# Kernel optimization log

Measured on AMD Instinct MI355X. Metric: run time of the kernel, lower is better.

## Reference

```python
import jax, jax.numpy as jnp
import numpy as np

NC = 5  # num_clusters == unfold window size


def conv1x3(x, w, b):
    # x: (B, Cin, H, W); w: (Cout, Cin, 1, 3); padding (0,1) like torch Conv2d
    y = jax.lax.conv_general_dilated(
        x, w, window_strides=(1, 1), padding=((0, 0), (1, 1)),
        dimension_numbers=("NCHW", "OIHW", "NCHW"))
    return y + b[None, :, None, None]


def setup_inputs() -> dict:
    key = jax.random.key(0)
    ks = jax.random.split(key, 8)
    b, h, l, d = 8, 8, 1024, 64
    dm = h * d  # d_model = 512
    f32 = jnp.float32
    s_conv1 = 1.0 / np.sqrt(dm * 3)
    s_conv2 = 1.0 / np.sqrt(NC * 3)
    s_lin = 1.0 / np.sqrt(NC)
    return {
        "Q": jax.random.normal(ks[0], (b, h, l, d), f32),
        "K": jax.random.normal(ks[1], (b, h, l, d), f32),
        "V": jax.random.normal(ks[2], (b, h, l, d), f32),
        "w_proj_k": jax.random.normal(ks[3], (NC, dm, 1, 3), f32) * s_conv1,
        "b_proj_k": jnp.zeros((NC,), f32),
        "w_proj_back": jax.random.normal(ks[4], (dm, NC, 1, 3), f32) * s_conv2,
        "b_proj_back": jnp.zeros((dm,), f32),
        "w_ck": jax.random.normal(ks[5], (NC, NC), f32) * s_lin,
        "b_ck": jnp.zeros((NC,), f32),
        "w_cq": jax.random.normal(ks[6], (NC, NC), f32) * s_lin,
        "b_cq": jnp.zeros((NC,), f32),
    }


def reference(Q, K, V, w_proj_k, b_proj_k, w_proj_back, b_proj_back,
              w_ck, b_ck, w_cq, b_cq):
    b, h, l, d = Q.shape
    u = NC  # unfolding window
    # --- padded unfold along batch dim: window i is K_padded[i:i+u] ---
    K_padded = jnp.concatenate(
        [jnp.zeros((u, h, l, d), Q.dtype), K[1:]], axis=0)  # (u+b-1, h, l, d)
    idx = jnp.arange(b)[:, None] + jnp.arange(u)[None, :]     # (b, u)
    Kw = K_padded[idx]                                        # (b, u, h, l, d)
    Kw = jnp.transpose(Kw, (0, 2, 3, 4, 1))                   # (b, h, l, d, u) == torch unfold layout
    K_unfold = Kw.reshape(b, h * d, l, u)                     # raw reshape, matches torch
    # --- project to clusters ---
    ckp = jax.nn.relu(conv1x3(K_unfold, w_proj_k, b_proj_k))  # (b, NC, l, u)
    ckp = jnp.transpose(ckp, (0, 2, 3, 1))                    # (b, l, u, NC)
    cluster_k = jax.nn.softmax(ckp @ w_ck.T + b_ck, axis=-1)
    cluster_q = jax.nn.softmax(ckp @ w_cq.T + b_cq, axis=-1)
    # --- distributional loss ---
    mu = jnp.mean(cluster_q, axis=-1)                         # (b, l, u)
    sigma = jax.nn.softplus(jnp.std(cluster_q, axis=-1, ddof=1))  # unbiased std like torch
    x = jnp.mean(cluster_k, axis=-1)
    log_prob = -0.5 * ((x - mu) / sigma) ** 2 - jnp.log(sigma) - 0.5 * jnp.log(2 * jnp.pi)
    # CrossEntropyLoss(mu, mu): class dim is axis=1 (l); soft-label targets = mu
    ce = -jnp.mean(jnp.sum(mu * jax.nn.log_softmax(mu, axis=1), axis=1))
    loss = -jnp.mean(log_prob) + ce
    # --- masked triangular cluster attention ---
    scores = jnp.einsum('blpc,bluc->blpu', cluster_q, cluster_k) / u  # (b, l, u, u)
    mask = jnp.triu(jnp.ones((u, u), bool), k=1)
    scores = jnp.where(mask, -1e9, scores)
    attn = jax.nn.softmax(scores, axis=-1)
    cluster_q2 = jnp.einsum('blpu,bluc->blpc', attn, cluster_q)       # (b, l, u, NC)
    # --- project back & second attention ---
    cc = jax.nn.relu(conv1x3(jnp.transpose(cluster_q2, (0, 3, 1, 2)),
                             w_proj_back, b_proj_back))               # (b, h*d, l, u)
    cluster_center = cc.reshape(b, h, u, l, d)                        # raw reshape, matches torch
    scores_center = jnp.einsum('bhqd,bhckd->bhqk', Q, cluster_center) # sums over c and d
    attn2 = jax.nn.softmax(scores_center, axis=-1)
    context = jnp.einsum('bhqk,bhkd->bhqd', attn2, V)
    return (context, loss)
```

## Files before the change

### kernel.cpp

```cpp
#include <hip/hip_runtime.h>
#include <math.h>

#define L 1024
#define D 64
#define H 8
#define B 8

#define WS_G    0
#define WS_MU   107520
#define WS_Q2   148480
#define WS_DSC_BYTE   1413120u
#define WS_KHI_BYTE   1413632u
#define WS_KLO_BYTE   9802240u
#define WS_NOV_END    18190848u
#define WS_VTHI_BYTE  18190848u
#define WS_VTLO_BYTE  26579456u
#define WS_V_END      34968064u

typedef __attribute__((ext_vector_type(8))) short bf16x8;
typedef __attribute__((ext_vector_type(4))) float f32x4;

__device__ __forceinline__ ushort f2bf(float x) {
  unsigned b = __builtin_bit_cast(unsigned, x);
  return (ushort)((b + 0x7FFFu + ((b >> 16) & 1u)) >> 16);
}
__device__ __forceinline__ float bf2f(ushort u) {
  unsigned t = ((unsigned)u) << 16;
  return __builtin_bit_cast(float, t);
}

__global__ __launch_bounds__(256) void k_part(const float* __restrict__ K,
                                              const float* __restrict__ wpk,
                                              float* __restrict__ G) {
  const int tid = threadIdx.x, lane = tid & 63, wid = tid >> 6;
  const int lq = blockIdx.x;
  const int bip = blockIdx.y + 1;
  __shared__ float w_s[512 * 16];
  __shared__ float red[3][64][16];
  for (int i = tid; i < 512 * 16; i += 256) {
    int c = i >> 4, f = i & 15;
    w_s[i] = (f < 15) ? wpk[((f / 3) * 512 + c) * 3 + (f % 3)] : 0.f;
  }
  __syncthreads();
  float acc[15];
#pragma unroll
  for (int f = 0; f < 15; ++f) acc[f] = 0.f;
  const float* Kb = K + (size_t)bip * (H * L * D);
  const int c0 = wid * 128;
#pragma unroll 4
  for (int c = c0; c < c0 + 128; ++c) {
    float val = Kb[((c >> 6) * L + ((c & 63) << 4) + lq) * D + lane];
    const float4* wr = (const float4*)&w_s[c * 16];
    float4 w0 = wr[0], w1 = wr[1], w2 = wr[2], w3 = wr[3];
    acc[0] = fmaf(val, w0.x, acc[0]);  acc[1] = fmaf(val, w0.y, acc[1]);
    acc[2] = fmaf(val, w0.z, acc[2]);  acc[3] = fmaf(val, w0.w, acc[3]);
    acc[4] = fmaf(val, w1.x, acc[4]);  acc[5] = fmaf(val, w1.y, acc[5]);
    acc[6] = fmaf(val, w1.z, acc[6]);  acc[7] = fmaf(val, w1.w, acc[7]);
    acc[8] = fmaf(val, w2.x, acc[8]);  acc[9] = fmaf(val, w2.y, acc[9]);
    acc[10] = fmaf(val, w2.z, acc[10]); acc[11] = fmaf(val, w2.w, acc[11]);
    acc[12] = fmaf(val, w3.x, acc[12]); acc[13] = fmaf(val, w3.y, acc[13]);
    acc[14] = fmaf(val, w3.z, acc[14]);
  }
  if (wid) {
#pragma unroll
    for (int f = 0; f < 15; ++f) red[wid - 1][lane][f] = acc[f];
  }
  __syncthreads();
  if (wid == 0) {
#pragma unroll
    for (int f = 0; f < 15; ++f)
      acc[f] += red[0][lane][f] + red[1][lane][f] + red[2][lane][f];
    float* dst = G + ((size_t)blockIdx.y * 1024 + (lq << 6) + lane) * 15;
#pragma unroll
    for (int f = 0; f < 15; ++f) dst[f] = acc[f];
  }
}

__global__ __launch_bounds__(256) void k_chain(const float* __restrict__ G,
    const float* __restrict__ b_pk, const float* __restrict__ w_ck,
    const float* __restrict__ b_ck, const float* __restrict__ w_cq,
    const float* __restrict__ b_cq, float* __restrict__ mu_out,
    float* __restrict__ q2_out, double* __restrict__ dsc) {
  int g = blockIdx.x * 256 + threadIdx.x;
  int bi = g >> 10, li = g & 1023;
  float ckp[5][5];
#pragma unroll
  for (int j = 0; j < 5; ++j) {
#pragma unroll
    for (int nc = 0; nc < 5; ++nc) {
      float s = b_pk[nc];
#pragma unroll
      for (int t = 0; t < 3; ++t) {
        int w = j + t - 1;
        int bip = bi + w - 4;
        if (w >= 0 && w < 5 && bip >= 1)
          s += G[(size_t)((bip - 1) * 1024 + li) * 15 + nc * 3 + t];
      }
      ckp[j][nc] = fmaxf(s, 0.f);
    }
  }
  float cq[5][5], ck[5][5];
  float lp_sum = 0.f;
#pragma unroll
  for (int j = 0; j < 5; ++j) {
    float vk[5], vq[5];
#pragma unroll
    for (int m = 0; m < 5; ++m) {
      float sk = b_ck[m], sq = b_cq[m];
#pragma unroll
      for (int n = 0; n < 5; ++n) {
        sk = fmaf(ckp[j][n], w_ck[m * 5 + n], sk);
        sq = fmaf(ckp[j][n], w_cq[m * 5 + n], sq);
      }
      vk[m] = sk; vq[m] = sq;
    }
    float mk = vk[0], mq = vq[0];
#pragma unroll
    for (int m = 1; m < 5; ++m) { mk = fmaxf(mk, vk[m]); mq = fmaxf(mq, vq[m]); }
    float sk = 0.f, sq = 0.f;
#pragma unroll
    for (int m = 0; m < 5; ++m) {
      vk[m] = expf(vk[m] - mk); sk += vk[m];
      vq[m] = expf(vq[m] - mq); sq += vq[m];
    }
    float rk = 1.f / sk, rq = 1.f / sq;
    float mu = 0.f, x = 0.f;
#pragma unroll
    for (int m = 0; m < 5; ++m) {
      ck[j][m] = vk[m] * rk; cq[j][m] = vq[m] * rq;
      mu += cq[j][m]; x += ck[j][m];
    }
    mu *= 0.2f; x *= 0.2f;
    float var = 0.f;
#pragma unroll
    for (int m = 0; m < 5; ++m) { float d0 = cq[j][m] - mu; var += d0 * d0; }
    var *= 0.25f;
    float sg = log1pf(expf(sqrtf(var)));
    float z = (x - mu) / sg;
    lp_sum += -0.5f * z * z - logf(sg) - 0.91893853320467274f;
    mu_out[(size_t)g * 5 + j] = mu;
  }
  float* q2p = q2_out + (size_t)g * 25;
#pragma unroll
  for (int pp = 0; pp < 5; ++pp) {
    float sc[5]; float mx = -3.0e38f;
    for (int u2 = 0; u2 <= pp; ++u2) {
      float d0 = 0.f;
#pragma unroll
      for (int c = 0; c < 5; ++c) d0 = fmaf(cq[pp][c], ck[u2][c], d0);
      sc[u2] = d0 * 0.2f;
      mx = fmaxf(mx, sc[u2]);
    }
    float den = 0.f;
    for (int u2 = 0; u2 <= pp; ++u2) { sc[u2] = expf(sc[u2] - mx); den += sc[u2]; }
    float rd = 1.f / den;
    float q2v[5] = {0.f, 0.f, 0.f, 0.f, 0.f};
    for (int u2 = 0; u2 <= pp; ++u2) {
      float a = sc[u2] * rd;
#pragma unroll
      for (int c = 0; c < 5; ++c) q2v[c] = fmaf(a, cq[u2][c], q2v[c]);
    }
#pragma unroll
    for (int c = 0; c < 5; ++c) q2p[pp * 5 + c] = q2v[c];
  }
  for (int off = 1; off < 64; off <<= 1) lp_sum += __shfl_xor(lp_sum, off, 64);
  __shared__ float wsum[4];
  int tid = threadIdx.x;
  if ((tid & 63) == 0) wsum[tid >> 6] = lp_sum;
  __syncthreads();
  if (tid == 0) atomicAdd(dsc, (double)(wsum[0] + wsum[1] + wsum[2] + wsum[3]));
}

__global__ __launch_bounds__(256) void k_ce(const float* __restrict__ mu,
                                            double* __restrict__ dsc) {
  int bi = blockIdx.x / 5, u = blockIdx.x % 5;
  int tid = threadIdx.x;
  const float* base = mu + (size_t)bi * L * 5 + u;
  float v[4];
#pragma unroll
  for (int k = 0; k < 4; ++k) v[k] = base[(tid + 256 * k) * 5];
  float mx = fmaxf(fmaxf(v[0], v[1]), fmaxf(v[2], v[3]));
  for (int off = 1; off < 64; off <<= 1) mx = fmaxf(mx, __shfl_xor(mx, off, 64));
  __shared__ float sh[4];
  if ((tid & 63) == 0) sh[tid >> 6] = mx;
  __syncthreads();
  mx = fmaxf(fmaxf(sh[0], sh[1]), fmaxf(sh[2], sh[3]));
  __syncthreads();
  float se = 0.f;
#pragma unroll
  for (int k = 0; k < 4; ++k) se += expf(v[k] - mx);
  for (int off = 1; off < 64; off <<= 1) se += __shfl_xor(se, off, 64);
  if ((tid & 63) == 0) sh[tid >> 6] = se;
  __syncthreads();
  float lse = mx + logf(sh[0] + sh[1] + sh[2] + sh[3]);
  __syncthreads();
  float part = 0.f;
#pragma unroll
  for (int k = 0; k < 4; ++k) part += v[k] * (v[k] - lse);
  for (int off = 1; off < 64; off <<= 1) part += __shfl_xor(part, off, 64);
  if ((tid & 63) == 0) sh[tid >> 6] = part;
  __syncthreads();
  if (tid == 0) atomicAdd(dsc + 1, (double)(sh[0] + sh[1] + sh[2] + sh[3]));
}

__global__ __launch_bounds__(256) void k_kprep(const float* __restrict__ q2,
    const float* __restrict__ wb, const float* __restrict__ bb,
    ushort* __restrict__ Khi_g, ushort* __restrict__ Klo_g) {
  int g = blockIdx.x * 256 + threadIdx.x;
  int bi = g >> 19;
  int r = g & 524287;
  int hh = r >> 16;
  int li = (r >> 6) & 1023;
  int dd = r & 63;
  int base = hh * 327680 + li * 64 + dd;
  const float* q2b = q2 + (size_t)bi * L * 25;
  float sum = 0.f;
#pragma unroll
  for (int cc = 0; cc < 5; ++cc) {
    int flat = base + cc * 65536;
    int co = (int)((unsigned)flat / 5120u);
    int rem = flat - co * 5120;
    int li2 = (int)((unsigned)rem / 5u);
    int j = rem - li2 * 5;
    const float* qr = q2b + li2 * 25;
    const float* wr = wb + co * 15;
    float s = bb[co];
#pragma unroll
    for (int t = 0; t < 3; ++t) {
      int w = j + t - 1;
      if (w >= 0 && w < 5) {
#pragma unroll
        for (int c = 0; c < 5; ++c) s = fmaf(qr[w * 5 + c], wr[c * 3 + t], s);
      }
    }
    sum += fmaxf(s, 0.f);
  }
  int kt = li >> 6, key = li & 63, c = dd >> 2, e = dd & 3;
  int idx = (((bi * 8 + hh) * 16 + kt) << 12) + (key << 6) + ((c ^ (key & 15)) << 2) + e;
  ushort hb = f2bf(sum);
  Khi_g[idx] = hb;
  Klo_g[idx] = f2bf(sum - bf2f(hb));
}

__global__ __launch_bounds__(256) void k_vprep(const float* __restrict__ V,
    ushort* __restrict__ Vthi_g, ushort* __restrict__ Vtlo_g) {
  __shared__ float t[64][65];
  const int tile = blockIdx.x;
  const float* Vb = V + ((size_t)tile << 12);
  const int tid = threadIdx.x;
  {
    int key = tid >> 2, c0 = (tid & 3) << 4;
#pragma unroll
    for (int i = 0; i < 4; ++i) {
      float4 v = *(const float4*)(Vb + key * 64 + c0 + 4 * i);
      t[key][c0 + 4 * i + 0] = v.x; t[key][c0 + 4 * i + 1] = v.y;
      t[key][c0 + 4 * i + 2] = v.z; t[key][c0 + 4 * i + 3] = v.w;
    }
  }
  __syncthreads();
  int d = tid >> 2, q4 = tid & 3;
#pragma unroll
  for (int q = 0; q < 4; ++q) {
    int kc = q4 * 4 + q;
    ushort hv[4], lv[4];
#pragma unroll
    for (int e = 0; e < 4; ++e) {
      float x = t[kc * 4 + e][d];
      ushort hb = f2bf(x);
      hv[e] = hb;
      lv[e] = f2bf(x - bf2f(hb));
    }
    int idx = (tile << 12) + (d << 6) + ((kc ^ (d & 15)) << 2);
    ushort4 h4; h4.x = hv[0]; h4.y = hv[1]; h4.z = hv[2]; h4.w = hv[3];
    ushort4 l4; l4.x = lv[0]; l4.y = lv[1]; l4.z = lv[2]; l4.w = lv[3];
    *(ushort4*)(&Vthi_g[idx]) = h4;
    *(ushort4*)(&Vtlo_g[idx]) = l4;
  }
}

template<bool VPREP>
__global__ __launch_bounds__(256) void k_attn(const float* __restrict__ Q,
    const ushort* __restrict__ Khi_g, const ushort* __restrict__ Klo_g,
    const ushort* __restrict__ Vthi_g, const ushort* __restrict__ Vtlo_g,
    const float* __restrict__ V, float* __restrict__ Out) {
  __shared__ ushort smem[2][16384];
  const int tid = threadIdx.x;
  const int lane = tid & 63;
  const int w = tid >> 6;
  const int lq = lane & 15;
  const int g = lane >> 4;
  const int id = blockIdx.x;
  const int bh = ((id & 7) << 3) + (id >> 6);
  const int qb = (id >> 3) & 7;
  const int q0 = qb << 7;
  const float* Qb = Q + ((size_t)bh * L + q0 + w * 32) * D;
  const float* Vb = V + (size_t)bh * L * D;
  const int tb = bh * 16;

  int cx0 = ((g) ^ lq) << 2, cx1 = ((g + 4) ^ lq) << 2;
  int cx2 = ((g + 8) ^ lq) << 2, cx3 = ((g + 12) ^ lq) << 2;

  bf16x8 qh[2][2], qlo[2][2];
#pragma unroll
  for (int qs = 0; qs < 2; ++qs) {
    const float* Qr = Qb + (qs * 16 + lq) * D;
#pragma unroll
    for (int ds = 0; ds < 2; ++ds) {
      float4 x0 = *(const float4*)(Qr + 4 * g + 32 * ds);
      float4 x1 = *(const float4*)(Qr + 4 * g + 16 + 32 * ds);
      float xs[8] = {x0.x, x0.y, x0.z, x0.w, x1.x, x1.y, x1.z, x1.w};
      bf16x8 h, l;
#pragma unroll
      for (int j = 0; j < 8; ++j) {
        ushort hb = f2bf(xs[j]);
        h[j] = (short)hb;
        l[j] = (short)f2bf(xs[j] - bf2f(hb));
      }
      qh[qs][ds] = h; qlo[qs][ds] = l;
    }
  }

  const ushort* warr;
  int wdst;
  if (VPREP) {
    warr = (w == 0) ? Khi_g : (w == 1) ? Klo_g : (w == 2) ? Vthi_g : Vtlo_g;
    wdst = w << 12;
  } else {
    warr = ((w < 2) ? Khi_g : Klo_g);
    wdst = ((w >> 1) << 12) + ((w & 1) << 11);
  }

#define STAGE(buf_, kt_) do {                                                  \
    const ushort* src_ = warr + ((size_t)(tb + (kt_)) << 12) +                 \
                         (VPREP ? 0 : ((w & 1) << 11)) + lane * 8;             \
    ushort* dst_ = &smem[buf_][wdst];                                          \
    _Pragma("unroll")                                                          \
    for (int r_ = 0; r_ < (VPREP ? 8 : 4); ++r_) {                             \
      __builtin_amdgcn_global_load_lds(                                        \
        (const __attribute__((address_space(1))) unsigned int*)(src_ + r_ * 512), \
        (__attribute__((address_space(3))) unsigned int*)(dst_ + r_ * 512 + lane * 8), \
        16, 0, 0);                                                             \
    }                                                                          \
  } while (0)

  float4 vreg[2][2];
  const int kp = tid & 31, dblk = tid >> 5;
#define VLOAD(kt_) do {                                                        \
    const float* Vb2_ = Vb + ((size_t)(kt_) << 12);                            \
    _Pragma("unroll")                                                          \
    for (int kk_ = 0; kk_ < 2; ++kk_)                                          \
      _Pragma("unroll")                                                        \
      for (int i_ = 0; i_ < 2; ++i_)                                           \
        vreg[kk_][i_] = *(const float4*)(Vb2_ + (2 * kp + kk_) * 64 + dblk * 8 + 4 * i_); \
  } while (0)
#define VWRITE(nb_) do {                                                       \
    ushort vh_[2][8], vl_[2][8];                                               \
    _Pragma("unroll")                                                          \
    for (int kk_ = 0; kk_ < 2; ++kk_)                                          \
      _Pragma("unroll")                                                        \
      for (int i_ = 0; i_ < 2; ++i_) {                                         \
        float xs_[4] = {vreg[kk_][i_].x, vreg[kk_][i_].y, vreg[kk_][i_].z, vreg[kk_][i_].w}; \
        _Pragma("unroll")                                                      \
        for (int e_ = 0; e_ < 4; ++e_) {                                       \
          ushort hb_ = f2bf(xs_[e_]);                                          \
          vh_[kk_][4 * i_ + e_] = hb_;                                         \
          vl_[kk_][4 * i_ + e_] = f2bf(xs_[e_] - bf2f(hb_));                   \
        }                                                                      \
      }                                                                        \
    _Pragma("unroll")                                                          \
    for (int dd_ = 0; dd_ < 8; ++dd_) {                                        \
      int d_ = dblk * 8 + dd_;                                                 \
      int idx_ = (d_ << 6) + (((kp >> 1) ^ (d_ & 15)) << 2) + ((kp & 1) << 1); \
      ushort2 ph_; ph_.x = vh_[0][dd_]; ph_.y = vh_[1][dd_];                   \
      ushort2 pl_; pl_.x = vl_[0][dd_]; pl_.y = vl_[1][dd_];                   \
      *(ushort2*)(&smem[nb_][8192 + idx_]) = ph_;                              \
      *(ushort2*)(&smem[nb_][12288 + idx_]) = pl_;                             \
    }                                                                          \
  } while (0)

  f32x4 O_[2][4];
  float m_[2], l_[2];
#pragma unroll
  for (int qs = 0; qs < 2; ++qs) {
    m_[qs] = -3.0e38f; l_[qs] = 0.f;
#pragma unroll
    for (int d2 = 0; d2 < 4; ++d2) O_[qs][d2] = (f32x4){0.f, 0.f, 0.f, 0.f};
  }

  STAGE(0, 0);
  if (!VPREP) { VLOAD(0); VWRITE(0); }
  __syncthreads();

  int cur = 0;
  for (int kt = 0; kt < 16; ++kt) {
    if (kt < 15) {
      STAGE(cur ^ 1, kt + 1);
      if (!VPREP) VLOAD(kt + 1);
    }

    const ushort* Kh = &smem[cur][0];
    const ushort* Kl = &smem[cur][4096];
    const ushort* Vh = &smem[cur][8192];
    const ushort* Vl = &smem[cur][12288];

    f32x4 S[4][2];
#pragma unroll
    for (int ks = 0; ks < 4; ++ks)
#pragma unroll
      for (int qs = 0; qs < 2; ++qs) S[ks][qs] = (f32x4){0.f, 0.f, 0.f, 0.f};
#pragma unroll
    for (int ds = 0; ds < 2; ++ds) {
      int ca = ds ? cx2 : cx0, cb = ds ? cx3 : cx1;
#pragma unroll
      for (int ksub = 0; ksub < 4; ++ksub) {
        int base = (ksub * 16 + lq) * 64;
        ushort4 a0 = *(const ushort4*)(Kh + base + ca);
        ushort4 a1 = *(const ushort4*)(Kh + base + cb);
        ushort4 b0 = *(const ushort4*)(Kl + base + ca);
        ushort4 b1 = *(const ushort4*)(Kl + base + cb);
        bf16x8 kh = {(short)a0.x, (short)a0.y, (short)a0.z, (short)a0.w,
                     (short)a1.x, (short)a1.y, (short)a1.z, (short)a1.w};
        bf16x8 kl = {(short)b0.x, (short)b0.y, (short)b0.z, (short)b0.w,
                     (short)b1.x, (short)b1.y, (short)b1.z, (short)b1.w};
#pragma unroll
        for (int qs = 0; qs < 2; ++qs) {
          S[ksub][qs] = __builtin_amdgcn_mfma_f32_16x16x32_bf16(kh, qh[qs][ds], S[ksub][qs], 0, 0, 0);
          S[ksub][qs] = __builtin_amdgcn_mfma_f32_16x16x32_bf16(kh, qlo[qs][ds], S[ksub][qs], 0, 0, 0);
          S[ksub][qs] = __builtin_amdgcn_mfma_f32_16x16x32_bf16(kl, qh[qs][ds], S[ksub][qs], 0, 0, 0);
        }
      }
    }

    bf16x8 pfh[2][2];
    float scl[2];
#pragma unroll
    for (int qs = 0; qs < 2; ++qs) {
      float tmax = -3.0e38f;
#pragma unroll
      for (int ks = 0; ks < 4; ++ks)
#pragma unroll
        for (int r = 0; r < 4; ++r) tmax = fmaxf(tmax, S[ks][qs][r]);
      tmax = fmaxf(tmax, __shfl_xor(tmax, 16, 64));
      tmax = fmaxf(tmax, __shfl_xor(tmax, 32, 64));
      float mn = fmaxf(m_[qs], tmax);
      scl[qs] = __expf(m_[qs] - mn);
      float p[4][4]; float rs = 0.f;
#pragma unroll
      for (int ks = 0; ks < 4; ++ks)
#pragma unroll
        for (int r = 0; r < 4; ++r) {
          float pv = __expf(S[ks][qs][r] - mn);
          p[ks][r] = pv; rs += pv;
        }
      rs += __shfl_xor(rs, 16, 64);
      rs += __shfl_xor(rs, 32, 64);
      l_[qs] = l_[qs] * scl[qs] + rs;
      m_[qs] = mn;
#pragma unroll
      for (int kst = 0; kst < 2; ++kst) {
        bf16x8 h;
#pragma unroll
        for (int jh = 0; jh < 2; ++jh)
#pragma unroll
          for (int j2 = 0; j2 < 4; ++j2)
            h[jh * 4 + j2] = (short)f2bf(p[jh + 2 * kst][j2]);
        pfh[qs][kst] = h;
      }
#pragma unroll
      for (int d2 = 0; d2 < 4; ++d2)
#pragma unroll
        for (int r = 0; r < 4; ++r) O_[qs][d2][r] *= scl[qs];
    }

#pragma unroll
    for (int kst = 0; kst < 2; ++kst) {
      int ca = kst ? cx2 : cx0, cb = kst ? cx3 : cx1;
#pragma unroll
      for (int d2 = 0; d2 < 4; ++d2) {
        int base = (d2 * 16 + lq) * 64;
        ushort4 a0 = *(const ushort4*)(Vh + base + ca);
        ushort4 a1 = *(const ushort4*)(Vh + base + cb);
        ushort4 b0 = *(const ushort4*)(Vl + base + ca);
        ushort4 b1 = *(const ushort4*)(Vl + base + cb);
        bf16x8 vh = {(short)a0.x, (short)a0.y, (short)a0.z, (short)a0.w,
                     (short)a1.x, (short)a1.y, (short)a1.z, (short)a1.w};
        bf16x8 vl = {(short)b0.x, (short)b0.y, (short)b0.z, (short)b0.w,
                     (short)b1.x, (short)b1.y, (short)b1.z, (short)b1.w};
#pragma unroll
        for (int qs = 0; qs < 2; ++qs) {
          O_[qs][d2] = __builtin_amdgcn_mfma_f32_16x16x32_bf16(vh, pfh[qs][kst], O_[qs][d2], 0, 0, 0);
          O_[qs][d2] = __builtin_amdgcn_mfma_f32_16x16x32_bf16(vl, pfh[qs][kst], O_[qs][d2], 0, 0, 0);
        }
      }
    }

    if (!VPREP && kt < 15) VWRITE(cur ^ 1);
    __syncthreads();
    cur ^= 1;
  }

  float* Ob = Out + ((size_t)bh * L + q0 + w * 32) * D;
#pragma unroll
  for (int qs = 0; qs < 2; ++qs) {
    float il = 1.f / l_[qs];
    int q = qs * 16 + lq;
#pragma unroll
    for (int d2 = 0; d2 < 4; ++d2) {
      float4 o4;
      o4.x = O_[qs][d2][0] * il; o4.y = O_[qs][d2][1] * il;
      o4.z = O_[qs][d2][2] * il; o4.w = O_[qs][d2][3] * il;
      *(float4*)(Ob + q * D + d2 * 16 + 4 * g) = o4;
    }
  }
#undef STAGE
#undef VLOAD
#undef VWRITE
}

__global__ void k_final(const double* __restrict__ dsc, float* __restrict__ out) {
  out[4194304] = (float)(-dsc[0] / 40960.0 - dsc[1] / 40.0);
}

extern "C" void kernel_launch(void* const* d_in, const int* in_sizes, int n_in,
                              void* d_out, int out_size, void* d_ws, size_t ws_size,
                              hipStream_t stream) {
  const float* Q   = (const float*)d_in[0];
  const float* K   = (const float*)d_in[1];
  const float* V   = (const float*)d_in[2];
  const float* wpk = (const float*)d_in[3];
  const float* bpk = (const float*)d_in[4];
  const float* wpb = (const float*)d_in[5];
  const float* bpb = (const float*)d_in[6];
  const float* wck = (const float*)d_in[7];
  const float* bck = (const float*)d_in[8];
  const float* wcq = (const float*)d_in[9];
  const float* bcq = (const float*)d_in[10];
  float* out = (float*)d_out;
  float* ws = (float*)d_ws;
  float* G    = ws + WS_G;
  float* mu   = ws + WS_MU;
  float* q2   = ws + WS_Q2;
  double* dsc = (double*)((char*)d_ws + WS_DSC_BYTE);
  ushort* Khi = (ushort*)((char*)d_ws + WS_KHI_BYTE);
  ushort* Klo = (ushort*)((char*)d_ws + WS_KLO_BYTE);
  ushort* Vthi = (ushort*)((char*)d_ws + WS_VTHI_BYTE);
  ushort* Vtlo = (ushort*)((char*)d_ws + WS_VTLO_BYTE);
  const bool vprep = (ws_size >= (size_t)WS_V_END);

  hipMemsetAsync((char*)d_ws + WS_DSC_BYTE, 0, 16, stream);
  if (vprep) k_vprep<<<1024, 256, 0, stream>>>(V, Vthi, Vtlo);
  k_part<<<dim3(16, 7), 256, 0, stream>>>(K, wpk, G);
  k_chain<<<32, 256, 0, stream>>>(G, bpk, wck, bck, wcq, bcq, mu, q2, dsc);
  k_ce<<<40, 256, 0, stream>>>(mu, dsc);
  k_kprep<<<16384, 256, 0, stream>>>(q2, wpb, bpb, Khi, Klo);
  if (vprep) {
    k_attn<true><<<512, 256, 0, stream>>>(Q, Khi, Klo, Vthi, Vtlo, V, out);
  } else {
    k_attn<false><<<512, 256, 0, stream>>>(Q, Khi, Klo, nullptr, nullptr, V, out);
  }
  k_final<<<1, 1, 0, stream>>>(dsc, out);
}
```

Before: 307.9 us.

## Split cluster back-projection into conv kernel with atomics and fold kernel

```diff
diff --git a/kernel.cpp b/kernel.cpp
--- a/kernel.cpp
+++ b/kernel.cpp
@@ -6,16 +6,16 @@
 #define H 8
 #define B 8
 
-#define WS_G    0
-#define WS_MU   107520
-#define WS_Q2   148480
-#define WS_DSC_BYTE   1413120u
-#define WS_KHI_BYTE   1413632u
-#define WS_KLO_BYTE   9802240u
-#define WS_NOV_END    18190848u
-#define WS_VTHI_BYTE  18190848u
-#define WS_VTLO_BYTE  26579456u
-#define WS_V_END      34968064u
+#define WS_G     0
+#define WS_MU    107520
+#define WS_Q2T   148480
+#define WS_Q2T_BYTE   593920u
+#define WS_DSC_BYTE   1740800u
+#define WS_KHI_BYTE   1740816u
+#define WS_KLO_BYTE   10129424u
+#define WS_VTHI_BYTE  18518032u
+#define WS_VTLO_BYTE  26906640u
+#define WS_V_END      35295248u
 
 typedef __attribute__((ext_vector_type(8))) short bf16x8;
 typedef __attribute__((ext_vector_type(4))) float f32x4;
@@ -80,7 +80,7 @@
     const float* __restrict__ b_pk, const float* __restrict__ w_ck,
     const float* __restrict__ b_ck, const float* __restrict__ w_cq,
     const float* __restrict__ b_cq, float* __restrict__ mu_out,
-    float* __restrict__ q2_out, double* __restrict__ dsc) {
+    float* __restrict__ q2t, double* __restrict__ dsc) {
   int g = blockIdx.x * 256 + threadIdx.x;
   int bi = g >> 10, li = g & 1023;
   float ckp[5][5];
@@ -140,7 +140,7 @@
     lp_sum += -0.5f * z * z - logf(sg) - 0.91893853320467274f;
     mu_out[(size_t)g * 5 + j] = mu;
   }
-  float* q2p = q2_out + (size_t)g * 25;
+  float* q2p = q2t + (((size_t)bi * 35) << 10) + li;
 #pragma unroll
   for (int pp = 0; pp < 5; ++pp) {
     float sc[5]; float mx = -3.0e38f;
@@ -161,7 +161,7 @@
       for (int c = 0; c < 5; ++c) q2v[c] = fmaf(a, cq[u2][c], q2v[c]);
     }
 #pragma unroll
-    for (int c = 0; c < 5; ++c) q2p[pp * 5 + c] = q2v[c];
+    for (int c = 0; c < 5; ++c) q2p[(size_t)(((pp + 1) * 5 + c)) << 10] = q2v[c];
   }
   for (int off = 1; off < 64; off <<= 1) lp_sum += __shfl_xor(lp_sum, off, 64);
   __shared__ float wsum[4];
@@ -203,40 +203,56 @@
   if (tid == 0) atomicAdd(dsc + 1, (double)(sh[0] + sh[1] + sh[2] + sh[3]));
 }
 
-__global__ __launch_bounds__(256) void k_kprep(const float* __restrict__ q2,
+__global__ __launch_bounds__(256) void k_cback(const float* __restrict__ q2t,
     const float* __restrict__ wb, const float* __restrict__ bb,
+    float* __restrict__ keff) {
+  __shared__ float ls[1280];
+  const int id = blockIdx.x;
+  const int bi = id >> 11, cog = (id >> 4) & 127, lt = id & 15;
+  const int tid = threadIdx.x, w = tid >> 6, lane = tid & 63;
+  const int co = cog * 4 + w;
+  const int li2 = (lt << 6) + lane;
+  const float* xb = q2t + (((size_t)bi * 35) << 10) + li2;
+  float xt[35];
+#pragma unroll
+  for (int k = 0; k < 35; ++k) xt[k] = xb[(size_t)k << 10];
+  float wbl[15];
+#pragma unroll
+  for (int t = 0; t < 3; ++t)
+#pragma unroll
+    for (int c = 0; c < 5; ++c) wbl[t * 5 + c] = wb[co * 15 + c * 3 + t];
+  const float bias = bb[co];
+#pragma unroll
+  for (int j = 0; j < 5; ++j) {
+    float s = bias;
+#pragma unroll
+    for (int i = 0; i < 15; ++i) s = fmaf(xt[j * 5 + i], wbl[i], s);
+    ls[w * 320 + lane * 5 + j] = fmaxf(s, 0.f);
+  }
+  __syncthreads();
+  const int base_lo = (cog * 4) * 5120 + (lt << 6) * 5;
+#pragma unroll
+  for (int k = 0; k < 5; ++k) {
+    int e = tid + (k << 8);
+    float val = ls[e];
+    int we = (int)((unsigned)e / 320u);
+    int off = e - we * 320;
+    int flat = base_lo + we * 5120 + off;
+    int q = flat >> 16;
+    int hh = (q * 205) >> 10;
+    int idx = (((bi << 3) + hh) << 16) + (flat & 65535);
+    atomicAdd(&keff[idx], val);
+  }
+}
+
+__global__ __launch_bounds__(256) void k_kfold(const float* __restrict__ keff,
     ushort* __restrict__ Khi_g, ushort* __restrict__ Klo_g) {
   int g = blockIdx.x * 256 + threadIdx.x;
-  int bi = g >> 19;
-  int r = g & 524287;
-  int hh = r >> 16;
-  int li = (r >> 6) & 1023;
-  int dd = r & 63;
-  int base = hh * 327680 + li * 64 + dd;
-  const float* q2b = q2 + (size_t)bi * L * 25;
-  float sum = 0.f;
-#pragma unroll
-  for (int cc = 0; cc < 5; ++cc) {
-    int flat = base + cc * 65536;
-    int co = (int)((unsigned)flat / 5120u);
-    int rem = flat - co * 5120;
-    int li2 = (int)((unsigned)rem / 5u);
-    int j = rem - li2 * 5;
-    const float* qr = q2b + li2 * 25;
-    const float* wr = wb + co * 15;
-    float s = bb[co];
-#pragma unroll
-    for (int t = 0; t < 3; ++t) {
-      int w = j + t - 1;
-      if (w >= 0 && w < 5) {
-#pragma unroll
-        for (int c = 0; c < 5; ++c) s = fmaf(qr[w * 5 + c], wr[c * 3 + t], s);
-      }
-    }
-    sum += fmaxf(s, 0.f);
-  }
+  float sum = keff[g];
+  int li = (g >> 6) & 1023, dd = g & 63;
+  int bh = g >> 16;
   int kt = li >> 6, key = li & 63, c = dd >> 2, e = dd & 3;
-  int idx = (((bi * 8 + hh) * 16 + kt) << 12) + (key << 6) + ((c ^ (key & 15)) << 2) + e;
+  int idx = ((bh * 16 + kt) << 12) + (key << 6) + ((c ^ (key & 15)) << 2) + e;
   ushort hb = f2bf(sum);
   Khi_g[idx] = hb;
   Klo_g[idx] = f2bf(sum - bf2f(hb));
@@ -539,20 +555,23 @@
   float* ws = (float*)d_ws;
   float* G    = ws + WS_G;
   float* mu   = ws + WS_MU;
-  float* q2   = ws + WS_Q2;
+  float* q2t  = ws + WS_Q2T;
   double* dsc = (double*)((char*)d_ws + WS_DSC_BYTE);
   ushort* Khi = (ushort*)((char*)d_ws + WS_KHI_BYTE);
   ushort* Klo = (ushort*)((char*)d_ws + WS_KLO_BYTE);
   ushort* Vthi = (ushort*)((char*)d_ws + WS_VTHI_BYTE);
   ushort* Vtlo = (ushort*)((char*)d_ws + WS_VTLO_BYTE);
   const bool vprep = (ws_size >= (size_t)WS_V_END);
-
-  hipMemsetAsync((char*)d_ws + WS_DSC_BYTE, 0, 16, stream);
+  float* keff = out;
+
+  hipMemsetAsync((char*)d_ws + WS_Q2T_BYTE, 0, (WS_DSC_BYTE - WS_Q2T_BYTE) + 16, stream);
+  hipMemsetAsync(out, 0, (size_t)4194304 * 4, stream);
   if (vprep) k_vprep<<<1024, 256, 0, stream>>>(V, Vthi, Vtlo);
   k_part<<<dim3(16, 7), 256, 0, stream>>>(K, wpk, G);
-  k_chain<<<32, 256, 0, stream>>>(G, bpk, wck, bck, wcq, bcq, mu, q2, dsc);
+  k_chain<<<32, 256, 0, stream>>>(G, bpk, wck, bck, wcq, bcq, mu, q2t, dsc);
   k_ce<<<40, 256, 0, stream>>>(mu, dsc);
-  k_kprep<<<16384, 256, 0, stream>>>(q2, wpb, bpb, Khi, Klo);
+  k_cback<<<16384, 256, 0, stream>>>(q2t, wpb, bpb, keff);
+  k_kfold<<<16384, 256, 0, stream>>>(keff, Khi, Klo);
   if (vprep) {
     k_attn<true><<<512, 256, 0, stream>>>(Q, Khi, Klo, Vthi, Vtlo, V, out);
   } else {
```

New measurement: 293.6 us. -4.6%, faster.
